# Performance work log

Hardware: AMD Instinct MI355X
Metric: run time of the kernel (lower is better)

Reference implementation:

```python
import jax, jax.numpy as jnp
import numpy as np

NEG_SLOPE = 0.2  # keras 'leaky_relu' default negative slope

def _leaky_relu(t):
    return jnp.where(t >= 0, t, NEG_SLOPE * t)

def setup_inputs() -> dict:
    key = jax.random.key(0)
    kx, kq, kk, kv, ko, kg = jax.random.split(key, 6)
    B, H, W, C, A = 4, 64, 64, 256, 128
    x = jax.random.normal(kx, (B, H, W, C), dtype=jnp.float32)
    # 1x1 conv kernels == [Cin, Cout] matrices; glorot-normal-ish scaling
    Wq = jax.random.normal(kq, (C, A), dtype=jnp.float32) * (2.0 / (C + A)) ** 0.5
    Wk = jax.random.normal(kk, (C, A), dtype=jnp.float32) * (2.0 / (C + A)) ** 0.5
    Wv = jax.random.normal(kv, (C, A), dtype=jnp.float32) * (2.0 / (C + A)) ** 0.5
    Wo = jax.random.normal(ko, (A, C), dtype=jnp.float32) * (2.0 / (A + C)) ** 0.5
    # ChannelLearnableMultiplier weight: truncated_normal(0, 0.01) ~ small values near 0
    w_gamma = jax.random.normal(kg, (1, 1, 1, C), dtype=jnp.float32) * 0.01
    return {"x": x, "Wq": Wq, "Wk": Wk, "Wv": Wv, "Wo": Wo, "w_gamma": w_gamma}

def reference(x, Wq, Wk, Wv, Wo, w_gamma):
    B, H, W, C = x.shape
    A = Wq.shape[1]
    # 1x1 conv projections with leaky_relu activation, flatten spatial -> [B, N, A]
    q = _leaky_relu(jnp.einsum('bhwc,ca->bhwa', x, Wq)).reshape(B, H * W, A)
    k = _leaky_relu(jnp.einsum('bhwc,ca->bhwa', x, Wk)).reshape(B, H * W, A)
    v = _leaky_relu(jnp.einsum('bhwc,ca->bhwa', x, Wv)).reshape(B, H * W, A)
    # keras Attention(use_scale=False, score_mode='dot'): softmax(q k^T) v
    scores = jnp.einsum('bnd,bmd->bnm', q, k)          # [B, N, N]
    attn = jax.nn.softmax(scores, axis=-1)
    o = jnp.einsum('bnm,bmd->bnd', attn, v)            # [B, N, A]
    o = o.reshape(B, H, W, A)
    # output 1x1 conv, linear activation
    y = jnp.einsum('bhwa,ac->bhwc', o, Wo)
    # ChannelLearnableMultiplier: tanh(relu(1 + w)) * y
    return jnp.tanh(jax.nn.relu(1.0 + w_gamma)) * y
```

## Files before the change

### kernel.cpp

```cpp
#include <hip/hip_runtime.h>
#include <hip/hip_bf16.h>
#include <cstdint>
#include <cstddef>

typedef __bf16 bf16x8 __attribute__((ext_vector_type(8)));
typedef _Float16 f16x8 __attribute__((ext_vector_type(8)));
typedef short short8 __attribute__((ext_vector_type(8)));
typedef short short4v __attribute__((ext_vector_type(4)));
typedef float f32x4 __attribute__((ext_vector_type(4)));

#if __has_builtin(__builtin_amdgcn_mfma_f32_16x16x16bf16_1k)
  #define HAVE_K16 1
  #define MFMA16BF(a,b,c) __builtin_amdgcn_mfma_f32_16x16x16bf16_1k((a),(b),(c),0,0,0)
#elif __has_builtin(__builtin_amdgcn_mfma_f32_16x16x16_bf16)
  #define HAVE_K16 1
  #define MFMA16BF(a,b,c) __builtin_amdgcn_mfma_f32_16x16x16_bf16((a),(b),(c),0,0,0)
#else
  #define HAVE_K16 0
#endif

__device__ __forceinline__ unsigned short f2bf(float f) {
    union { float f; uint32_t u; } v; v.f = f;
    uint32_t u = v.u;
    return (unsigned short)((u + 0x7FFFu + ((u >> 16) & 1u)) >> 16);
}
__device__ __forceinline__ float bf2f(unsigned short h) {
    union { uint32_t u; float f; } v; v.u = ((uint32_t)h) << 16;
    return v.f;
}
__device__ __forceinline__ unsigned short f2h(float f) {
    union { _Float16 h; unsigned short u; } v; v.h = (_Float16)f;
    return v.u;
}

__global__ __launch_bounds__(256) void prep_kernel(
    const float* __restrict__ Wq, const float* __restrict__ Wk,
    const float* __restrict__ Wv, const float* __restrict__ Wo,
    const float* __restrict__ wg,
    unsigned short* __restrict__ wt_hi,
    unsigned short* __restrict__ wt_lo,
    unsigned short* __restrict__ wot,
    float* __restrict__ gamma)
{
    const int bid = blockIdx.x, t = threadIdx.x;
    __shared__ __align__(16) unsigned short Th[128][72], Tl[128][72];
    if (bid < 12) {
        const int proj = bid >> 2, kc = bid & 3;
        const float* W = (proj == 0) ? Wq : ((proj == 1) ? Wk : Wv);
        for (int r = 0; r < 32; ++r) {
            int idx = r * 256 + t;
            int kk = idx >> 7, n = idx & 127;
            float w = W[(size_t)(kc * 64 + kk) * 128 + n];
            unsigned short h = f2bf(w);
            Th[n][kk] = h;
            Tl[n][kk] = f2bf(w - bf2f(h));
        }
        __syncthreads();
        int n = t >> 1, k0 = (t & 1) * 32;
        size_t off = (size_t)proj * 32768 + (size_t)kc * 8192 + (size_t)n * 64 + k0;
        #pragma unroll
        for (int j = 0; j < 4; ++j) {
            *(short8*)(wt_hi + off + j * 8) = *(const short8*)(&Th[n][k0 + j * 8]);
            *(short8*)(wt_lo + off + j * 8) = *(const short8*)(&Tl[n][k0 + j * 8]);
        }
    } else if (bid < 16) {
        const int c0 = (bid - 12) * 64;
        unsigned short* T = &Th[0][0];
        for (int r = 0; r < 32; ++r) {
            int idx = r * 256 + t;
            int a = idx >> 6, cc = idx & 63;
            T[cc * 136 + a] = f2bf(Wo[(size_t)a * 256 + c0 + cc]);
        }
        __syncthreads();
        int cc = t >> 2, a0 = (t & 3) * 32;
        #pragma unroll
        for (int j = 0; j < 4; ++j)
            *(short8*)(wot + (size_t)(c0 + cc) * 128 + a0 + j * 8) =
                *(const short8*)(&T[cc * 136 + a0 + j * 8]);
    } else {
        float g = 1.0f + wg[t];
        if (g < 0.f) g = 0.f;
        gamma[t] = tanhf(g);
    }
}

__global__ __launch_bounds__(256) void qkv_kernel(
    const float* __restrict__ x,
    const unsigned short* __restrict__ wt_hi,
    const unsigned short* __restrict__ wt_lo,
    unsigned short* __restrict__ qkv_ws)
{
    const int rowtile = blockIdx.x;
    const int proj    = blockIdx.y;
    unsigned short* outqk = qkv_ws + (size_t)proj * 2097152u;
    unsigned short* vt    = qkv_ws + (size_t)2 * 2097152u;
    const bool need_lo = (proj < 2);

    const int tid  = threadIdx.x;
    const int lane = tid & 63, wave = tid >> 6;
    const int lo   = lane & 15, quad = lane >> 4;

    __shared__ __align__(16) unsigned short Xh[64][72], Xl[64][72];
    __shared__ __align__(16) unsigned short Wh[128][72], Wl[128][72];

    f32x4 acc[8];
    #pragma unroll
    for (int i = 0; i < 8; ++i) acc[i] = (f32x4){0.f, 0.f, 0.f, 0.f};

    const int wn = tid >> 1, wk0 = (tid & 1) * 32;

    for (int kc = 0; kc < 4; ++kc) {
        __syncthreads();
        #pragma unroll
        for (int i = 0; i < 4; ++i) {
            int flat4 = (i * 256 + tid) * 4;
            int row = flat4 >> 6, col = flat4 & 63;
            float4 tv4 = *(const float4*)(x + (size_t)(rowtile * 64 + row) * 256 + kc * 64 + col);
            float tv[4] = {tv4.x, tv4.y, tv4.z, tv4.w};
            short4v h, l;
            #pragma unroll
            for (int j = 0; j < 4; ++j) {
                unsigned short hj = f2bf(tv[j]);
                h[j] = (short)hj;
                l[j] = (short)f2bf(tv[j] - bf2f(hj));
            }
            *(short4v*)(&Xh[row][col]) = h;
            if (need_lo) *(short4v*)(&Xl[row][col]) = l;
        }
        {
            const size_t off = (size_t)proj * 32768 + (size_t)kc * 8192 + (size_t)wn * 64 + wk0;
            #pragma unroll
            for (int j = 0; j < 4; ++j)
                *(short8*)(&Wh[wn][wk0 + j * 8]) = *(const short8*)(wt_hi + off + j * 8);
            if (need_lo) {
                #pragma unroll
                for (int j = 0; j < 4; ++j)
                    *(short8*)(&Wl[wn][wk0 + j * 8]) = *(const short8*)(wt_lo + off + j * 8);
            }
        }
        __syncthreads();
        #pragma unroll
        for (int ks = 0; ks < 2; ++ks) {
            bf16x8 ah = *(const bf16x8*)(&Xh[wave * 16 + lo][ks * 32 + quad * 8]);
            #pragma unroll
            for (int nb = 0; nb < 8; ++nb) {
                bf16x8 bh = *(const bf16x8*)(&Wh[nb * 16 + lo][ks * 32 + quad * 8]);
                acc[nb] = __builtin_amdgcn_mfma_f32_16x16x32_bf16(ah, bh, acc[nb], 0, 0, 0);
                if (need_lo) {
                    bf16x8 al = *(const bf16x8*)(&Xl[wave * 16 + lo][ks * 32 + quad * 8]);
                    bf16x8 bl = *(const bf16x8*)(&Wl[nb * 16 + lo][ks * 32 + quad * 8]);
                    acc[nb] = __builtin_amdgcn_mfma_f32_16x16x32_bf16(al, bh, acc[nb], 0, 0, 0);
                    acc[nb] = __builtin_amdgcn_mfma_f32_16x16x32_bf16(ah, bl, acc[nb], 0, 0, 0);
                }
            }
        }
    }
    if (proj < 2) {
        #pragma unroll
        for (int nb = 0; nb < 8; ++nb) {
            #pragma unroll
            for (int r = 0; r < 4; ++r) {
                float v = acc[nb][r];
                v = (v >= 0.f) ? v : 0.2f * v;
                int m = rowtile * 64 + wave * 16 + quad * 4 + r;
                outqk[(size_t)m * 128 + nb * 16 + lo] = f2h(v);
            }
        }
    } else {
        const int b  = rowtile >> 6;
        const int sb = (rowtile & 63) * 64;
        #pragma unroll
        for (int nb = 0; nb < 8; ++nb) {
            #pragma unroll
            for (int r = 0; r < 4; ++r) {
                float v = acc[nb][r];
                v = (v >= 0.f) ? v : 0.2f * v;
                int seq = sb + wave * 16 + quad * 4 + r;
                int d   = nb * 16 + lo;
                vt[(size_t)b * 524288 + (size_t)d * 4096 + seq] = f2bf(v);
            }
        }
    }
}

#if HAVE_K16
__global__ __launch_bounds__(256) void attn_kernel(
    const unsigned short* __restrict__ qkv_ws,
    unsigned short* __restrict__ part,
    float* __restrict__ lpart,
    int chunk)
{
    const int b  = blockIdx.x;
    const int qt = blockIdx.y;
    const int z  = blockIdx.z;
    const int tid  = threadIdx.x;
    const int lane = tid & 63, wave = tid >> 6;
    const int lo   = lane & 15, quad = lane >> 4;

    const unsigned short* q  = qkv_ws;
    const unsigned short* k  = qkv_ws + 2097152u;
    const unsigned short* vt = qkv_ws + (size_t)2 * 2097152u + (size_t)b * 524288u;

    __shared__ __align__(16) unsigned short Ks[32][136];
    __shared__ __align__(16) unsigned short Vt[128][40];

    const int qbase = qt * 128 + wave * 32;
    f16x8 qf[2][4];
    #pragma unroll
    for (int g = 0; g < 2; ++g)
        #pragma unroll
        for (int ks = 0; ks < 4; ++ks)
            qf[g][ks] = *(const f16x8*)(q + ((size_t)(b * 4096 + qbase + g * 16 + lo)) * 128
                                          + ks * 32 + quad * 8);

    f32x4 oacc[2][8];
    #pragma unroll
    for (int g = 0; g < 2; ++g)
        #pragma unroll
        for (int i = 0; i < 8; ++i) oacc[g][i] = (f32x4){0.f, 0.f, 0.f, 0.f};
    float Lsum[2] = {1e-30f, 1e-30f};

    const float LOG2E  = 1.44269504088896f;
    const float NSHIFT = -40.0f * 1.44269504088896f;

    const int krow0 = tid >> 4, kcol0 = (tid & 15) * 8;
    const int krow1 = 16 + (tid >> 4);
    const int vd = tid >> 2, vc = tid & 3;
    const int vst  = vc >> 1;
    const int colA = ((2 * vc) & 3) * 8 + vst * 4;
    const int colB = ((2 * vc + 1) & 3) * 8 + vst * 4;

    const int niter = chunk >> 5;
    const int sbase = z * chunk;

    short8 ka, kb, va, vb;
    ka = *(const short8*)(k + ((size_t)(b * 4096 + sbase + krow0)) * 128 + kcol0);
    kb = *(const short8*)(k + ((size_t)(b * 4096 + sbase + krow1)) * 128 + kcol0);
    va = *(const short8*)(vt + (size_t)vd * 4096 + sbase + vc * 8);
    vb = *(const short8*)(vt + (size_t)(vd + 64) * 4096 + sbase + vc * 8);

    for (int kt = 0; kt < niter; ++kt) {
        __syncthreads();
        *(short8*)(&Ks[krow0][kcol0]) = ka;
        *(short8*)(&Ks[krow1][kcol0]) = kb;
        {
            short4v a0 = {va[0], va[1], va[2], va[3]}, a1 = {va[4], va[5], va[6], va[7]};
            short4v b0 = {vb[0], vb[1], vb[2], vb[3]}, b1 = {vb[4], vb[5], vb[6], vb[7]};
            *(short4v*)(&Vt[vd][colA])      = a0;
            *(short4v*)(&Vt[vd][colB])      = a1;
            *(short4v*)(&Vt[vd + 64][colA]) = b0;
            *(short4v*)(&Vt[vd + 64][colB]) = b1;
        }
        __syncthreads();
        if (kt + 1 < niter) {
            const int s1 = sbase + (kt + 1) * 32;
            ka = *(const short8*)(k + ((size_t)(b * 4096 + s1 + krow0)) * 128 + kcol0);
            kb = *(const short8*)(k + ((size_t)(b * 4096 + s1 + krow1)) * 128 + kcol0);
            va = *(const short8*)(vt + (size_t)vd * 4096 + s1 + vc * 8);
            vb = *(const short8*)(vt + (size_t)(vd + 64) * 4096 + s1 + vc * 8);
        }

        f32x4 sT[2][2];
        sT[0][0] = (f32x4){0.f,0.f,0.f,0.f}; sT[0][1] = (f32x4){0.f,0.f,0.f,0.f};
        sT[1][0] = (f32x4){0.f,0.f,0.f,0.f}; sT[1][1] = (f32x4){0.f,0.f,0.f,0.f};
        #pragma unroll
        for (int ks = 0; ks < 4; ++ks) {
            #pragma unroll
            for (int st = 0; st < 2; ++st) {
                f16x8 kf = *(const f16x8*)(&Ks[st * 16 + lo][ks * 32 + quad * 8]);
                sT[0][st] = __builtin_amdgcn_mfma_f32_16x16x32_f16(kf, qf[0][ks], sT[0][st], 0, 0, 0);
                sT[1][st] = __builtin_amdgcn_mfma_f32_16x16x32_f16(kf, qf[1][ks], sT[1][st], 0, 0, 0);
            }
        }
        short4v Pp[2][2];
        #pragma unroll
        for (int g = 0; g < 2; ++g) {
            #pragma unroll
            for (int st = 0; st < 2; ++st) {
                #pragma unroll
                for (int r = 0; r < 4; ++r) {
                    float t = fminf(fmaf(sT[g][st][r], LOG2E, NSHIFT), 125.0f);
                    union { float f; uint32_t u; } pv; pv.f = exp2f(t);
                    unsigned short pt = (unsigned short)(pv.u >> 16);
                    Lsum[g] += bf2f(pt);
                    Pp[g][st][r] = (short)pt;
                }
            }
        }
        #pragma unroll
        for (int nb = 0; nb < 8; ++nb) {
            short8 vv = *(const short8*)(&Vt[nb * 16 + lo][quad * 8]);
            short4v v0 = {vv[0], vv[1], vv[2], vv[3]};
            short4v v1 = {vv[4], vv[5], vv[6], vv[7]};
            #pragma unroll
            for (int g = 0; g < 2; ++g) {
                oacc[g][nb] = MFMA16BF(Pp[g][0], v0, oacc[g][nb]);
                oacc[g][nb] = MFMA16BF(Pp[g][1], v1, oacc[g][nb]);
            }
        }
    }

    #pragma unroll
    for (int g = 0; g < 2; ++g) {
        float xr = Lsum[g];
        xr += __shfl_xor(xr, 16, 64);
        xr += __shfl_xor(xr, 32, 64);
        Lsum[g] = xr;
    }
    #pragma unroll
    for (int g = 0; g < 2; ++g) {
        #pragma unroll
        for (int nb = 0; nb < 8; ++nb) {
            #pragma unroll
            for (int r = 0; r < 4; ++r) {
                int m = b * 4096 + qbase + g * 16 + quad * 4 + r;
                part[((size_t)z * 16384 + m) * 128 + nb * 16 + lo] = f2bf(oacc[g][nb][r]);
            }
        }
        if (lane < 16) {
            int m = b * 4096 + qbase + g * 16 + lane;
            lpart[(size_t)z * 16384 + m] = Lsum[g];
        }
    }
}
#else
__global__ __launch_bounds__(256) void attn_kernel(
    const unsigned short* __restrict__ qkv_ws,
    unsigned short* __restrict__ part,
    float* __restrict__ lpart,
    int chunk)
{
    const int b  = blockIdx.x;
    const int qt = blockIdx.y;
    const int z  = blockIdx.z;
    const int tid  = threadIdx.x;
    const int lane = tid & 63, wave = tid >> 6;
    const int lo   = lane & 15, quad = lane >> 4;

    const unsigned short* q  = qkv_ws;
    const unsigned short* k  = qkv_ws + 2097152u;
    const unsigned short* vt = qkv_ws + (size_t)2 * 2097152u + (size_t)b * 524288u;

    __shared__ __align__(16) unsigned short Ks[32][136];
    __shared__ __align__(16) unsigned short Vt[128][40];
    __shared__ __align__(16) unsigned short Ps[4][32][40];

    const int qbase = qt * 128 + wave * 32;
    f16x8 qf[2][4];
    #pragma unroll
    for (int g = 0; g < 2; ++g)
        #pragma unroll
        for (int ks = 0; ks < 4; ++ks)
            qf[g][ks] = *(const f16x8*)(q + ((size_t)(b * 4096 + qbase + g * 16 + lo)) * 128
                                          + ks * 32 + quad * 8);
    f32x4 oacc[2][8];
    #pragma unroll
    for (int g = 0; g < 2; ++g)
        #pragma unroll
        for (int i = 0; i < 8; ++i) oacc[g][i] = (f32x4){0.f, 0.f, 0.f, 0.f};
    float lsum[2][4];
    #pragma unroll
    for (int g = 0; g < 2; ++g)
        #pragma unroll
        for (int r = 0; r < 4; ++r) lsum[g][r] = 1e-30f;

    const float LOG2E  = 1.44269504088896f;
    const float NSHIFT = -40.0f * 1.44269504088896f;

    const int krow0 = tid >> 4, kcol0 = (tid & 15) * 8;
    const int krow1 = 16 + (tid >> 4);
    const int vd0 = tid >> 2, vs0 = (tid & 3) * 8;

    const int niter = chunk >> 5;
    const int sbase = z * chunk;

    short8 ka, kb, va, vb;
    ka = *(const short8*)(k + ((size_t)(b * 4096 + sbase + krow0)) * 128 + kcol0);
    kb = *(const short8*)(k + ((size_t)(b * 4096 + sbase + krow1)) * 128 + kcol0);
    va = *(const short8*)(vt + (size_t)vd0 * 4096 + sbase + vs0);
    vb = *(const short8*)(vt + (size_t)(vd0 + 64) * 4096 + sbase + vs0);

    for (int kt = 0; kt < niter; ++kt) {
        __syncthreads();
        *(short8*)(&Ks[krow0][kcol0]) = ka;
        *(short8*)(&Ks[krow1][kcol0]) = kb;
        *(short8*)(&Vt[vd0][vs0]) = va;
        *(short8*)(&Vt[vd0 + 64][vs0]) = vb;
        __syncthreads();
        if (kt + 1 < niter) {
            const int s1 = sbase + (kt + 1) * 32;
            ka = *(const short8*)(k + ((size_t)(b * 4096 + s1 + krow0)) * 128 + kcol0);
            kb = *(const short8*)(k + ((size_t)(b * 4096 + s1 + krow1)) * 128 + kcol0);
            va = *(const short8*)(vt + (size_t)vd0 * 4096 + s1 + vs0);
            vb = *(const short8*)(vt + (size_t)(vd0 + 64) * 4096 + s1 + vs0);
        }
        f32x4 s[2][2];
        s[0][0] = (f32x4){0.f,0.f,0.f,0.f}; s[0][1] = (f32x4){0.f,0.f,0.f,0.f};
        s[1][0] = (f32x4){0.f,0.f,0.f,0.f}; s[1][1] = (f32x4){0.f,0.f,0.f,0.f};
        #pragma unroll
        for (int ks = 0; ks < 4; ++ks) {
            #pragma unroll
            for (int nb = 0; nb < 2; ++nb) {
                f16x8 bf = *(const f16x8*)(&Ks[nb * 16 + lo][ks * 32 + quad * 8]);
                s[0][nb] = __builtin_amdgcn_mfma_f32_16x16x32_f16(qf[0][ks], bf, s[0][nb], 0, 0, 0);
                s[1][nb] = __builtin_amdgcn_mfma_f32_16x16x32_f16(qf[1][ks], bf, s[1][nb], 0, 0, 0);
            }
        }
        #pragma unroll
        for (int g = 0; g < 2; ++g)
            #pragma unroll
            for (int nb = 0; nb < 2; ++nb)
                #pragma unroll
                for (int r = 0; r < 4; ++r) {
                    float t = fminf(fmaf(s[g][nb][r], LOG2E, NSHIFT), 125.0f);
                    union { float f; uint32_t u; } pv; pv.f = exp2f(t);
                    unsigned short pt = (unsigned short)(pv.u >> 16);
                    lsum[g][r] += bf2f(pt);
                    Ps[wave][g * 16 + quad * 4 + r][nb * 16 + lo] = pt;
                }
        bf16x8 pf0 = *(const bf16x8*)(&Ps[wave][lo][quad * 8]);
        bf16x8 pf1 = *(const bf16x8*)(&Ps[wave][16 + lo][quad * 8]);
        #pragma unroll
        for (int nb = 0; nb < 8; ++nb) {
            bf16x8 vf = *(const bf16x8*)(&Vt[nb * 16 + lo][quad * 8]);
            oacc[0][nb] = __builtin_amdgcn_mfma_f32_16x16x32_bf16(pf0, vf, oacc[0][nb], 0, 0, 0);
            oacc[1][nb] = __builtin_amdgcn_mfma_f32_16x16x32_bf16(pf1, vf, oacc[1][nb], 0, 0, 0);
        }
    }
    #pragma unroll
    for (int g = 0; g < 2; ++g) {
        #pragma unroll
        for (int r = 0; r < 4; ++r) {
            float xr = lsum[g][r];
            #pragma unroll
            for (int m = 1; m < 16; m <<= 1) xr += __shfl_xor(xr, m, 64);
            lsum[g][r] = xr;
        }
        #pragma unroll
        for (int nb = 0; nb < 8; ++nb)
            #pragma unroll
            for (int r = 0; r < 4; ++r) {
                int m = b * 4096 + qbase + g * 16 + quad * 4 + r;
                part[((size_t)z * 16384 + m) * 128 + nb * 16 + lo] = f2bf(oacc[g][nb][r]);
            }
        if (lo == 0)
            #pragma unroll
            for (int r = 0; r < 4; ++r) {
                int m = b * 4096 + qbase + g * 16 + quad * 4 + r;
                lpart[(size_t)z * 16384 + m] = lsum[g][r];
            }
    }
}
#endif

__global__ __launch_bounds__(256) void outproj_kernel(
    const unsigned short* __restrict__ part,
    const float* __restrict__ lpart,
    const unsigned short* __restrict__ wot,
    const float* __restrict__ gamma,
    float* __restrict__ out,
    int nsplit)
{
    const int rowtile = blockIdx.x;
    const int tid  = threadIdx.x;
    const int lane = tid & 63, wave = tid >> 6;
    const int lo   = lane & 15, quad = lane >> 4;

    __shared__ __align__(16) unsigned short Os[64][136];
    __shared__ __align__(16) unsigned short WoT[128][136];

    #pragma unroll
    for (int i = 0; i < 4; ++i) {
        int flat = (i * 256 + tid) * 8;
        int row = flat >> 7, col = flat & 127;
        int m = rowtile * 64 + row;
        float acc8[8] = {0.f,0.f,0.f,0.f,0.f,0.f,0.f,0.f};
        float l = 0.f;
        for (int zz = 0; zz < nsplit; ++zz) {
            short8 t = *(const short8*)(part + ((size_t)zz * 16384 + m) * 128 + col);
            #pragma unroll
            for (int j = 0; j < 8; ++j) acc8[j] += bf2f((unsigned short)t[j]);
            l += lpart[(size_t)zz * 16384 + m];
        }
        float inv = 1.0f / l;
        short8 o8;
        #pragma unroll
        for (int j = 0; j < 8; ++j) o8[j] = (short)f2bf(acc8[j] * inv);
        *(short8*)(&Os[row][col]) = o8;
    }

    const int wc = tid >> 1, wa0 = (tid & 1) * 64;
    for (int ch = 0; ch < 2; ++ch) {
        if (ch) __syncthreads();
        #pragma unroll
        for (int j = 0; j < 8; ++j)
            *(short8*)(&WoT[wc][wa0 + j * 8]) =
                *(const short8*)(wot + (size_t)(ch * 128 + wc) * 128 + wa0 + j * 8);
        __syncthreads();

        f32x4 acc[8];
        #pragma unroll
        for (int i = 0; i < 8; ++i) acc[i] = (f32x4){0.f, 0.f, 0.f, 0.f};
        #pragma unroll
        for (int ks = 0; ks < 4; ++ks) {
            bf16x8 a = *(const bf16x8*)(&Os[wave * 16 + lo][ks * 32 + quad * 8]);
            #pragma unroll
            for (int nb = 0; nb < 8; ++nb) {
                bf16x8 bf = *(const bf16x8*)(&WoT[nb * 16 + lo][ks * 32 + quad * 8]);
                acc[nb] = __builtin_amdgcn_mfma_f32_16x16x32_bf16(a, bf, acc[nb], 0, 0, 0);
            }
        }
        #pragma unroll
        for (int nb = 0; nb < 8; ++nb) {
            int c = ch * 128 + nb * 16 + lo;
            float g = gamma[c];
            #pragma unroll
            for (int r = 0; r < 4; ++r) {
                int m = rowtile * 64 + wave * 16 + quad * 4 + r;
                out[(size_t)m * 256 + c] = acc[nb][r] * g;
            }
        }
    }
}

extern "C" void kernel_launch(void* const* d_in, const int* in_sizes, int n_in,
                              void* d_out, int out_size, void* d_ws, size_t ws_size,
                              hipStream_t stream) {
    const float* x  = (const float*)d_in[0];
    const float* Wq = (const float*)d_in[1];
    const float* Wk = (const float*)d_in[2];
    const float* Wv = (const float*)d_in[3];
    const float* Wo = (const float*)d_in[4];
    const float* wg = (const float*)d_in[5];
    float* out = (float*)d_out;

    unsigned short* ws = (unsigned short*)d_ws;
    const int nsplit = (ws_size >= (size_t)47000000) ? 8 : 4;
    const int chunk  = 4096 / nsplit;

    unsigned short* qkv_ws = ws;
    unsigned short* part   = ws + (size_t)3 * 2097152u;
    unsigned short* wt_hi  = part;
    unsigned short* wt_lo  = part + 98304u;
    float* lpart = (float*)(part + (size_t)nsplit * 2097152u);
    unsigned short* wot = (unsigned short*)(lpart + (size_t)nsplit * 16384u);
    float* gamma = (float*)(wot + 32768u);

    prep_kernel<<<dim3(17), 256, 0, stream>>>(Wq, Wk, Wv, Wo, wg, wt_hi, wt_lo, wot, gamma);
    qkv_kernel<<<dim3(256, 3), 256, 0, stream>>>(x, wt_hi, wt_lo, qkv_ws);
    attn_kernel<<<dim3(4, 32, nsplit), 256, 0, stream>>>(qkv_ws, part, lpart, chunk);
    outproj_kernel<<<dim3(256), 256, 0, stream>>>(part, lpart, wot, gamma, out, nsplit);
}
```

Measured before the change: 178.1 us.

## Double-buffer K/V shared tiles and software-pipeline PV MFMA with QK

Splits the K and V shared-memory tiles into two buffers. The P·V MFMAs for the previous tile now run while the current tile's QK scores are computed, and the next tile's shared-memory stores and global prefetch are interleaved with them. This aims to overlap exp/softmax work with matrix ops and reduce the exposed stall at each barrier. It also swaps exp2f for the native amdgcn exp2 builtin, which skips range handling. The cost is doubled shared memory per block and more live registers, since Pp is carried across iterations.

New measurement: 170.7 us. 1.04x faster.

```diff
diff --git a/kernel.cpp b/kernel.cpp
--- a/kernel.cpp
+++ b/kernel.cpp
@@ -17,6 +17,12 @@
   #define MFMA16BF(a,b,c) __builtin_amdgcn_mfma_f32_16x16x16_bf16((a),(b),(c),0,0,0)
 #else
   #define HAVE_K16 0
+#endif
+
+#if __has_builtin(__builtin_amdgcn_exp2f)
+  #define EXP2F(x) __builtin_amdgcn_exp2f(x)
+#else
+  #define EXP2F(x) exp2f(x)
 #endif
 
 __device__ __forceinline__ unsigned short f2bf(float f) {
@@ -201,8 +207,8 @@
     const unsigned short* k  = qkv_ws + 2097152u;
     const unsigned short* vt = qkv_ws + (size_t)2 * 2097152u + (size_t)b * 524288u;
 
-    __shared__ __align__(16) unsigned short Ks[32][136];
-    __shared__ __align__(16) unsigned short Vt[128][40];
+    __shared__ __align__(16) unsigned short Ks[2][32][136];
+    __shared__ __align__(16) unsigned short Vt[2][128][40];
 
     const int qbase = qt * 128 + wave * 32;
     f16x8 qf[2][4];
@@ -238,27 +244,29 @@
     kb = *(const short8*)(k + ((size_t)(b * 4096 + sbase + krow1)) * 128 + kcol0);
     va = *(const short8*)(vt + (size_t)vd * 4096 + sbase + vc * 8);
     vb = *(const short8*)(vt + (size_t)(vd + 64) * 4096 + sbase + vc * 8);
+    *(short8*)(&Ks[0][krow0][kcol0]) = ka;
+    *(short8*)(&Ks[0][krow1][kcol0]) = kb;
+    {
+        short4v a0 = {va[0], va[1], va[2], va[3]}, a1 = {va[4], va[5], va[6], va[7]};
+        short4v b0 = {vb[0], vb[1], vb[2], vb[3]}, b1 = {vb[4], vb[5], vb[6], vb[7]};
+        *(short4v*)(&Vt[0][vd][colA])      = a0;
+        *(short4v*)(&Vt[0][vd][colB])      = a1;
+        *(short4v*)(&Vt[0][vd + 64][colA]) = b0;
+        *(short4v*)(&Vt[0][vd + 64][colB]) = b1;
+    }
+    if (1 < niter) {
+        const int s1 = sbase + 32;
+        ka = *(const short8*)(k + ((size_t)(b * 4096 + s1 + krow0)) * 128 + kcol0);
+        kb = *(const short8*)(k + ((size_t)(b * 4096 + s1 + krow1)) * 128 + kcol0);
+        va = *(const short8*)(vt + (size_t)vd * 4096 + s1 + vc * 8);
+        vb = *(const short8*)(vt + (size_t)(vd + 64) * 4096 + s1 + vc * 8);
+    }
+    __syncthreads();
+
+    short4v Pp[2][2];
 
     for (int kt = 0; kt < niter; ++kt) {
-        __syncthreads();
-        *(short8*)(&Ks[krow0][kcol0]) = ka;
-        *(short8*)(&Ks[krow1][kcol0]) = kb;
-        {
-            short4v a0 = {va[0], va[1], va[2], va[3]}, a1 = {va[4], va[5], va[6], va[7]};
-            short4v b0 = {vb[0], vb[1], vb[2], vb[3]}, b1 = {vb[4], vb[5], vb[6], vb[7]};
-            *(short4v*)(&Vt[vd][colA])      = a0;
-            *(short4v*)(&Vt[vd][colB])      = a1;
-            *(short4v*)(&Vt[vd + 64][colA]) = b0;
-            *(short4v*)(&Vt[vd + 64][colB]) = b1;
-        }
-        __syncthreads();
-        if (kt + 1 < niter) {
-            const int s1 = sbase + (kt + 1) * 32;
-            ka = *(const short8*)(k + ((size_t)(b * 4096 + s1 + krow0)) * 128 + kcol0);
-            kb = *(const short8*)(k + ((size_t)(b * 4096 + s1 + krow1)) * 128 + kcol0);
-            va = *(const short8*)(vt + (size_t)vd * 4096 + s1 + vc * 8);
-            vb = *(const short8*)(vt + (size_t)(vd + 64) * 4096 + s1 + vc * 8);
-        }
+        const int cur = kt & 1, oth = cur ^ 1;
 
         f32x4 sT[2][2];
         sT[0][0] = (f32x4){0.f,0.f,0.f,0.f}; sT[0][1] = (f32x4){0.f,0.f,0.f,0.f};
@@ -267,12 +275,42 @@
         for (int ks = 0; ks < 4; ++ks) {
             #pragma unroll
             for (int st = 0; st < 2; ++st) {
-                f16x8 kf = *(const f16x8*)(&Ks[st * 16 + lo][ks * 32 + quad * 8]);
+                f16x8 kf = *(const f16x8*)(&Ks[cur][st * 16 + lo][ks * 32 + quad * 8]);
                 sT[0][st] = __builtin_amdgcn_mfma_f32_16x16x32_f16(kf, qf[0][ks], sT[0][st], 0, 0, 0);
                 sT[1][st] = __builtin_amdgcn_mfma_f32_16x16x32_f16(kf, qf[1][ks], sT[1][st], 0, 0, 0);
             }
         }
-        short4v Pp[2][2];
+        if (kt > 0) {
+            #pragma unroll
+            for (int nb = 0; nb < 8; ++nb) {
+                short8 vv = *(const short8*)(&Vt[oth][nb * 16 + lo][quad * 8]);
+                short4v v0 = {vv[0], vv[1], vv[2], vv[3]};
+                short4v v1 = {vv[4], vv[5], vv[6], vv[7]};
+                #pragma unroll
+                for (int g = 0; g < 2; ++g) {
+                    oacc[g][nb] = MFMA16BF(Pp[g][0], v0, oacc[g][nb]);
+                    oacc[g][nb] = MFMA16BF(Pp[g][1], v1, oacc[g][nb]);
+                }
+            }
+        }
+        __syncthreads();
+        if (kt + 1 < niter) {
+            *(short8*)(&Ks[oth][krow0][kcol0]) = ka;
+            *(short8*)(&Ks[oth][krow1][kcol0]) = kb;
+            short4v a0 = {va[0], va[1], va[2], va[3]}, a1 = {va[4], va[5], va[6], va[7]};
+            short4v b0 = {vb[0], vb[1], vb[2], vb[3]}, b1 = {vb[4], vb[5], vb[6], vb[7]};
+            *(short4v*)(&Vt[oth][vd][colA])      = a0;
+            *(short4v*)(&Vt[oth][vd][colB])      = a1;
+            *(short4v*)(&Vt[oth][vd + 64][colA]) = b0;
+            *(short4v*)(&Vt[oth][vd + 64][colB]) = b1;
+        }
+        if (kt + 2 < niter) {
+            const int s2 = sbase + (kt + 2) * 32;
+            ka = *(const short8*)(k + ((size_t)(b * 4096 + s2 + krow0)) * 128 + kcol0);
+            kb = *(const short8*)(k + ((size_t)(b * 4096 + s2 + krow1)) * 128 + kcol0);
+            va = *(const short8*)(vt + (size_t)vd * 4096 + s2 + vc * 8);
+            vb = *(const short8*)(vt + (size_t)(vd + 64) * 4096 + s2 + vc * 8);
+        }
         #pragma unroll
         for (int g = 0; g < 2; ++g) {
             #pragma unroll
@@ -280,16 +318,20 @@
                 #pragma unroll
                 for (int r = 0; r < 4; ++r) {
                     float t = fminf(fmaf(sT[g][st][r], LOG2E, NSHIFT), 125.0f);
-                    union { float f; uint32_t u; } pv; pv.f = exp2f(t);
+                    union { float f; uint32_t u; } pv; pv.f = EXP2F(t);
                     unsigned short pt = (unsigned short)(pv.u >> 16);
                     Lsum[g] += bf2f(pt);
                     Pp[g][st][r] = (short)pt;
                 }
             }
         }
+        __syncthreads();
+    }
+    {
+        const int last = (niter - 1) & 1;
         #pragma unroll
         for (int nb = 0; nb < 8; ++nb) {
-            short8 vv = *(const short8*)(&Vt[nb * 16 + lo][quad * 8]);
+            short8 vv = *(const short8*)(&Vt[last][nb * 16 + lo][quad * 8]);
             short4v v0 = {vv[0], vv[1], vv[2], vv[3]};
             short4v v1 = {vv[4], vv[5], vv[6], vv[7]};
             #pragma unroll
@@ -413,7 +455,7 @@
                 #pragma unroll
                 for (int r = 0; r < 4; ++r) {
                     float t = fminf(fmaf(s[g][nb][r], LOG2E, NSHIFT), 125.0f);
-                    union { float f; uint32_t u; } pv; pv.f = exp2f(t);
+                    union { float f; uint32_t u; } pv; pv.f = EXP2F(t);
                     unsigned short pt = (unsigned short)(pv.u >> 16);
                     lsum[g][r] += bf2f(pt);
                     Ps[wave][g * 16 + quad * 4 + r][nb * 16 + lo] = pt;
```
